# Kernel tuning notes

Measured on AMD Instinct MI355X. Metric: run time of the kernel, lower is better.

The kernel has to match this reference:

```python
import jax, jax.numpy as jnp
import numpy as np
import math

B, S, D, H = 64, 512, 768, 12
HS = D // H  # head size = 64


def setup_inputs() -> dict:
    key = jax.random.key(0)
    ks = jax.random.split(key, 8)
    scale = 1.0 / math.sqrt(D)
    return {
        "from_tensor": jax.random.normal(ks[0], (B, S, D), jnp.float32),
        "to_tensor": jax.random.normal(ks[1], (B, S, D), jnp.float32),
        "Wq": jax.random.normal(ks[2], (D, D), jnp.float32) * scale,
        "bq": jax.random.normal(ks[3], (D,), jnp.float32) * 0.02,
        "Wk": jax.random.normal(ks[4], (D, D), jnp.float32) * scale,
        "bk": jax.random.normal(ks[5], (D,), jnp.float32) * 0.02,
        "Wv": jax.random.normal(ks[6], (D, D), jnp.float32) * scale,
        "bv": jax.random.normal(ks[7], (D,), jnp.float32) * 0.02,
    }


def _split_heads(x):
    # [B, S, D] -> [B, H, S, HS]
    return x.reshape(B, S, H, HS).transpose(0, 2, 1, 3)


def reference(from_tensor, to_tensor, Wq, bq, Wk, bk, Wv, bv):
    q = _split_heads(from_tensor @ Wq + bq)
    k = _split_heads(to_tensor @ Wk + bk)
    v = _split_heads(to_tensor @ Wv + bv)
    scores = jnp.einsum("bhqd,bhkd->bhqk", q, k) / math.sqrt(HS)
    probs = jax.nn.softmax(scores, axis=-1)
    out = jnp.einsum("bhqk,bhkd->bhqd", probs, v)
    return out.transpose(0, 2, 1, 3).reshape(B, S, D)
```

## Files before the change

### kernel.cpp

```cpp
#include <hip/hip_runtime.h>
#include <hip/hip_bf16.h>

#define GAS __attribute__((address_space(1)))
#define LAS __attribute__((address_space(3)))

typedef __attribute__((ext_vector_type(8))) short   bf16x8;
typedef __attribute__((ext_vector_type(4))) float   f32x4;
typedef __attribute__((ext_vector_type(16))) float  f32x16;
typedef __attribute__((ext_vector_type(4))) float   f4;
typedef __attribute__((ext_vector_type(8))) short   s8v;
typedef __attribute__((ext_vector_type(2))) unsigned int u32x2;
typedef __attribute__((ext_vector_type(4))) unsigned int u32x4;

#define NB  64
#define NS  512
#define ND  768
#define NH  12
#define NHS 64
#define NM  (NB*NS)

#define QSCALE 0.18033688011112042f

__device__ __forceinline__ unsigned short f2bf(float x){
  unsigned int u = __float_as_uint(x);
  u += 0x7fffu + ((u >> 16) & 1u);
  return (unsigned short)(u >> 16);
}

__device__ __forceinline__ f32x4 mfma16(bf16x8 a, bf16x8 b, f32x4 c){
  return __builtin_amdgcn_mfma_f32_16x16x32_bf16(a, b, c, 0, 0, 0);
}

__device__ __forceinline__ f32x16 mfma32(bf16x8 a, bf16x8 b, f32x16 c){
  return __builtin_amdgcn_mfma_f32_32x32x16_bf16(a, b, c, 0, 0, 0);
}

__device__ __forceinline__ unsigned int cvtpk(float lo, float hi){
  unsigned int r;
  asm("v_cvt_pk_bf16_f32 %0, %1, %2" : "=v"(r) : "v"(lo), "v"(hi));
  return r;
}

__device__ __forceinline__ bf16x8 u2b(u32x4 u){
  union { u32x4 a; bf16x8 b; } c; c.a = u; return c.b;
}

__global__ void cvt_all(const float* __restrict__ from_t, const float* __restrict__ to_t,
                        const float* __restrict__ Wq, const float* __restrict__ Wk,
                        const float* __restrict__ Wv,
                        short* __restrict__ fb, short* __restrict__ tb,
                        short* __restrict__ Wt){
  int bid = blockIdx.x;
  if (bid < 24576){
    int v = bid * 256 + threadIdx.x;
    const int NG = NM * ND / 8;
    const float* s; short* d;
    if (v < NG){ s = from_t; d = fb; } else { s = to_t; d = tb; v -= NG; }
    f4 a = ((const f4*)s)[(long)v * 2];
    f4 b = ((const f4*)s)[(long)v * 2 + 1];
    s8v o;
    o[0]=(short)f2bf(a[0]); o[1]=(short)f2bf(a[1]); o[2]=(short)f2bf(a[2]); o[3]=(short)f2bf(a[3]);
    o[4]=(short)f2bf(b[0]); o[5]=(short)f2bf(b[1]); o[6]=(short)f2bf(b[2]); o[7]=(short)f2bf(b[3]);
    ((s8v*)d)[v] = o;
  } else {
    int i = (bid - 24576) * 256 + threadIdx.x;
    int mat = i / (ND*ND);
    int rem = i - mat * (ND*ND);
    int k = rem / ND;
    int n = rem - k * ND;
    const float* W = (mat == 0) ? Wq : (mat == 1 ? Wk : Wv);
    Wt[(long)mat*ND*ND + (long)n*ND + k] = (short)f2bf(W[rem]);
  }
}

__global__ __launch_bounds__(512, 2)
void qkv_gemm(const short* __restrict__ Xf, const short* __restrict__ Xt,
              const short* __restrict__ Wt,
              const float* __restrict__ bq, const float* __restrict__ bk,
              const float* __restrict__ bv,
              short* __restrict__ Qw, short* __restrict__ Kw, short* __restrict__ Vtw){
  __shared__ short smem[49152];

  int bid = blockIdx.x;
  int wg  = (bid & 7) * 144 + (bid >> 3);
  int mat = wg / 384;
  int r   = wg - mat * 384;
  int mt  = r / 3;
  int nt  = r - mt * 3;

  const short* A  = (mat == 0) ? Xf : Xt;
  const short* Wp = Wt + (long)mat * ND * ND;

  int t_ = threadIdx.x, wv = t_ >> 6, l = t_ & 63, g = l >> 4, c = l & 15;
  int wm = wv >> 2, wn = wv & 3;
  int m0 = mt * 256, n0 = nt * 256;

  short* As[3] = { smem, smem + 8192, smem + 16384 };
  short* Bs[3] = { smem + 24576, smem + 32768, smem + 40960 };

  auto stage = [&](int kt, short* Ab, short* Bb, int ci){
    int chunk = ci * 8 + wv;
    int ch = chunk & 15;
    int idx = ch * 64 + l;
    int row = idx >> 2, slot = idx & 3;
    int kcol = kt * 32 + ((slot ^ ((row >> 1) & 3)) << 3);
    if (chunk < 16){
      const short* gp = A + (long)(m0 + row) * ND + kcol;
      __builtin_amdgcn_global_load_lds((const GAS unsigned int*)gp,
                                       (LAS unsigned int*)(Ab + ch * 512), 16, 0, 0);
    } else {
      const short* gp = Wp + (long)(n0 + row) * ND + kcol;
      __builtin_amdgcn_global_load_lds((const GAS unsigned int*)gp,
                                       (LAS unsigned int*)(Bb + ch * 512), 16, 0, 0);
    }
  };

  f32x4 zero = {0.f, 0.f, 0.f, 0.f};
  f32x4 acc[8][4];
  #pragma unroll
  for (int i = 0; i < 8; ++i)
    #pragma unroll
    for (int j = 0; j < 4; ++j) acc[i][j] = zero;

  #pragma unroll
  for (int ci = 0; ci < 4; ++ci) stage(0, As[0], Bs[0], ci);
  #pragma unroll
  for (int ci = 0; ci < 4; ++ci) stage(1, As[1], Bs[1], ci);

  auto step = [&](const short* Asl, const short* Bsl, short* An, short* Bn, int t){
    if (t == 23) asm volatile("s_waitcnt vmcnt(0)" ::: "memory");
    else         asm volatile("s_waitcnt vmcnt(4)" ::: "memory");
    __builtin_amdgcn_s_barrier();
    bf16x8 af[8], bfv[4];
    #pragma unroll
    for (int ms = 0; ms < 4; ++ms){
      int row = wm * 128 + ms * 16 + c;
      af[ms] = *(const bf16x8*)(Asl + row * 32 + ((g ^ ((row >> 1) & 3)) << 3));
    }
    if (t < 22) stage(t + 2, An, Bn, 0);
    #pragma unroll
    for (int ns = 0; ns < 4; ++ns){
      int row = wn * 64 + ns * 16 + c;
      bfv[ns] = *(const bf16x8*)(Bsl + row * 32 + ((g ^ ((row >> 1) & 3)) << 3));
    }
    if (t < 22) stage(t + 2, An, Bn, 1);
    #pragma unroll
    for (int ms = 4; ms < 8; ++ms){
      int row = wm * 128 + ms * 16 + c;
      af[ms] = *(const bf16x8*)(Asl + row * 32 + ((g ^ ((row >> 1) & 3)) << 3));
    }
    if (t < 22){ stage(t + 2, An, Bn, 2); stage(t + 2, An, Bn, 3); }
    __builtin_amdgcn_s_setprio(1);
    #pragma unroll
    for (int ms = 0; ms < 8; ++ms)
      #pragma unroll
      for (int ns = 0; ns < 4; ++ns)
        acc[ms][ns] = mfma16(af[ms], bfv[ns], acc[ms][ns]);
    __builtin_amdgcn_s_setprio(0);
  };

  for (int it = 0; it < 8; ++it){
    int t = it * 3;
    step(As[0], Bs[0], As[2], Bs[2], t);
    step(As[1], Bs[1], As[0], Bs[0], t + 1);
    step(As[2], Bs[2], As[1], Bs[1], t + 2);
  }

  __builtin_amdgcn_s_barrier();

  int n0g = n0 + wn * 64;
  const float* bias = (mat == 0) ? bq : (mat == 1 ? bk : bv);
  float bb[4];
  #pragma unroll
  for (int ns = 0; ns < 4; ++ns) bb[ns] = bias[n0g + ns * 16 + c];
  short* chunk = smem + wv * 4096;
  int hq = n0g >> 6;

  if (mat < 2){
    short* O = (mat == 0) ? Qw : Kw;
    float scl = (mat == 0) ? QSCALE : 1.0f;
    #pragma unroll
    for (int sp = 0; sp < 2; ++sp){
      #pragma unroll
      for (int msl = 0; msl < 4; ++msl){
        #pragma unroll
        for (int ns = 0; ns < 4; ++ns){
          int col = ns * 16 + c;
          #pragma unroll
          for (int i = 0; i < 4; ++i){
            int row = msl * 16 + g * 4 + i;
            chunk[row * 64 + (((col >> 3) ^ (row & 7)) << 3) + (col & 7)] =
                (short)f2bf((acc[sp * 4 + msl][ns][i] + bb[ns]) * scl);
          }
        }
      }
      asm volatile("s_waitcnt lgkmcnt(0)" ::: "memory");
      __builtin_amdgcn_sched_barrier(0);
      #pragma unroll
      for (int rr = 0; rr < 8; ++rr){
        int row = rr * 8 + (l >> 3);
        int slot = l & 7;
        bf16x8 v = *(const bf16x8*)(chunk + row * 64 + ((slot ^ (row & 7)) << 3));
        int m = m0 + wm * 128 + sp * 64 + row;
        int b = m >> 9, s2 = m & 511;
        *(bf16x8*)(O + (((long)(b * NH + hq) * NS + s2) << 6) + slot * 8) = v;
      }
      if (sp == 0){ asm volatile("s_waitcnt lgkmcnt(0)" ::: "memory"); }
    }
  } else {
    #pragma unroll
    for (int sp = 0; sp < 2; ++sp){
      #pragma unroll
      for (int msl = 0; msl < 4; ++msl){
        #pragma unroll
        for (int ns = 0; ns < 4; ++ns){
          int hs = ns * 16 + c;
          #pragma unroll
          for (int i = 0; i < 4; ++i){
            int col = msl * 16 + g * 4 + i;
            chunk[hs * 64 + (((col >> 3) ^ (hs & 7)) << 3) + (col & 7)] =
                (short)f2bf(acc[sp * 4 + msl][ns][i] + bb[ns]);
          }
        }
      }
      asm volatile("s_waitcnt lgkmcnt(0)" ::: "memory");
      __builtin_amdgcn_sched_barrier(0);
      int mbase = m0 + wm * 128 + sp * 64;
      int b = mbase >> 9, s0 = mbase & 511;
      #pragma unroll
      for (int rr = 0; rr < 8; ++rr){
        int hs = rr * 8 + (l >> 3);
        int slot = l & 7;
        bf16x8 v = *(const bf16x8*)(chunk + hs * 64 + ((slot ^ (hs & 7)) << 3));
        *(bf16x8*)(Vtw + (long)((b * NH + hq) * 64 + hs) * NS + s0 + slot * 8) = v;
      }
      if (sp == 0){ asm volatile("s_waitcnt lgkmcnt(0)" ::: "memory"); }
    }
  }
}

__global__ __launch_bounds__(512, 1)
void attn_kernel(const short* __restrict__ Qw, const short* __restrict__ Kw,
                 const short* __restrict__ Vtw, float* __restrict__ out){
  extern __shared__ char smem[];
  short* Ks = (short*)smem;
  short* Vs = (short*)(smem + 65536);

  int bh = blockIdx.x;
  int t = threadIdx.x, wv = t >> 6, l = t & 63;
  int lam = l & 31, hi = l >> 5;
  int r7 = lam & 7;

  const short* Kb = Kw  + (long)bh * NS * NHS;
  const short* Vb = Vtw + (long)bh * NS * NHS;

  #pragma unroll
  for (int it = 0; it < 8; ++it){
    int chunk = it * 8 + wv;
    {
      int idx = chunk * 64 + l;
      int row = idx >> 3, slot = idx & 7;
      const short* gk = Kb + row * 64 + ((slot ^ (row & 7)) * 8);
      __builtin_amdgcn_global_load_lds((const GAS unsigned int*)gk,
                                       (LAS unsigned int*)(Ks + chunk * 512), 16, 0, 0);
    }
    {
      int row = chunk, slot = l;
      const short* gv = Vb + (long)row * NS + (((slot & 56) | ((slot & 7) ^ (row & 7))) * 8);
      __builtin_amdgcn_global_load_lds((const GAS unsigned int*)gv,
                                       (LAS unsigned int*)(Vs + chunk * 512), 16, 0, 0);
    }
  }
  __syncthreads();

  int b = bh / NH, h = bh - b * NH;
  float* outb = out + (long)b * NS * ND + (long)h * 64;

  for (int qt = 0; qt < 2; ++qt){
    int q0 = wv * 64 + qt * 32;
    const short* Qb = Qw + (((long)bh * NS + q0 + lam) << 6) + hi * 8;
    bf16x8 qf[4];
    #pragma unroll
    for (int dk = 0; dk < 4; ++dk) qf[dk] = *(const bf16x8*)(Qb + dk * 16);

    f32x16 o0, o1;
    #pragma unroll
    for (int j = 0; j < 16; ++j){ o0[j] = 0.f; o1[j] = 0.f; }
    float m_run = -1e30f, lsum = 0.f;

    f32x16 s2[2];
    bf16x8 kfr[2][4];
    {
      const char* kb = (const char*)Ks + lam * 128;
      #pragma unroll
      for (int dk = 0; dk < 4; ++dk)
        kfr[0][dk] = *(const bf16x8*)(kb + (((hi + 2 * dk) ^ r7) << 4));
      #pragma unroll
      for (int j = 0; j < 16; ++j) s2[0][j] = 0.f;
      __builtin_amdgcn_s_setprio(1);
      #pragma unroll
      for (int dk = 0; dk < 4; ++dk) s2[0] = mfma32(kfr[0][dk], qf[dk], s2[0]);
      __builtin_amdgcn_s_setprio(0);
    }

    #pragma unroll
    for (int ch = 0; ch < 16; ++ch){
      const int cur = ch & 1, nxt = cur ^ 1;

      if (ch < 15){
        const char* kb = (const char*)Ks + ((ch + 1) * 32 + lam) * 128;
        #pragma unroll
        for (int dk = 0; dk < 4; ++dk)
          kfr[nxt][dk] = *(const bf16x8*)(kb + (((hi + 2 * dk) ^ r7) << 4));
      }

      float t8[8], t4[4];
      #pragma unroll
      for (int j = 0; j < 8; ++j) t8[j] = fmaxf(s2[cur][j], s2[cur][j + 8]);
      #pragma unroll
      for (int j = 0; j < 4; ++j) t4[j] = fmaxf(t8[j], t8[j + 4]);
      float m1 = fmaxf(fmaxf(t4[0], t4[1]), fmaxf(t4[2], t4[3]));
      float pmax = fmaxf(m1, __shfl_xor(m1, 32));
      if (__any(pmax > m_run + 8.0f)){
        float mnew = fmaxf(m_run, pmax);
        float cf = exp2f(m_run - mnew);
        lsum *= cf;
        #pragma unroll
        for (int j = 0; j < 16; ++j){ o0[j] *= cf; o1[j] *= cf; }
        m_run = mnew;
      }
      float p[16];
      #pragma unroll
      for (int j = 0; j < 16; ++j) p[j] = exp2f(s2[cur][j] - m_run);
      float a8[8], a4[4];
      #pragma unroll
      for (int j = 0; j < 8; ++j) a8[j] = p[j] + p[j + 8];
      #pragma unroll
      for (int j = 0; j < 4; ++j) a4[j] = a8[j] + a8[j + 4];
      lsum += (a4[0] + a4[1]) + (a4[2] + a4[3]);

      if (ch < 15){
        #pragma unroll
        for (int j = 0; j < 16; ++j) s2[nxt][j] = 0.f;
        __builtin_amdgcn_s_setprio(1);
        #pragma unroll
        for (int dk = 0; dk < 4; ++dk) s2[nxt] = mfma32(kfr[nxt][dk], qf[dk], s2[nxt]);
        __builtin_amdgcn_s_setprio(0);
      }

      unsigned int w[8];
      #pragma unroll
      for (int rr = 0; rr < 8; ++rr) w[rr] = cvtpk(p[2 * rr], p[2 * rr + 1]);
      unsigned int y0 = (unsigned int)__shfl_xor((int)(hi ? w[0] : w[2]), 32);
      unsigned int y1 = (unsigned int)__shfl_xor((int)(hi ? w[1] : w[3]), 32);
      unsigned int y2 = (unsigned int)__shfl_xor((int)(hi ? w[4] : w[6]), 32);
      unsigned int y3 = (unsigned int)__shfl_xor((int)(hi ? w[5] : w[7]), 32);
      u32x4 fa, fb;
      if (hi){
        fa[0] = y0;   fa[1] = y1;   fa[2] = w[2]; fa[3] = w[3];
        fb[0] = y2;   fb[1] = y3;   fb[2] = w[6]; fb[3] = w[7];
      } else {
        fa[0] = w[0]; fa[1] = w[1]; fa[2] = y0;   fa[3] = y1;
        fb[0] = w[4]; fb[1] = w[5]; fb[2] = y2;   fb[3] = y3;
      }
      bf16x8 pa = u2b(fa), pb = u2b(fb);

      const char* vb0 = (const char*)Vs + lam * 1024;
      const char* vb1 = (const char*)Vs + (32 + lam) * 1024;
      int sl0 = ch * 4 + hi, sl1 = ch * 4 + 2 + hi;
      int sw0 = ((sl0 & 56) | ((sl0 & 7) ^ r7)) << 4;
      int sw1 = ((sl1 & 56) | ((sl1 & 7) ^ r7)) << 4;
      bf16x8 v00 = *(const bf16x8*)(vb0 + sw0);
      bf16x8 v01 = *(const bf16x8*)(vb0 + sw1);
      bf16x8 v10 = *(const bf16x8*)(vb1 + sw0);
      bf16x8 v11 = *(const bf16x8*)(vb1 + sw1);
      __builtin_amdgcn_s_setprio(1);
      o0 = mfma32(v00, pa, o0);
      o0 = mfma32(v01, pb, o0);
      o1 = mfma32(v10, pa, o1);
      o1 = mfma32(v11, pb, o1);
      __builtin_amdgcn_s_setprio(0);
    }

    float lt = lsum + __shfl_xor(lsum, 32);
    float invl = 1.0f / lt;
    float* orow = outb + (long)(q0 + lam) * ND;
    #pragma unroll
    for (int r = 0; r < 4; ++r){
      f4 u0, u1;
      #pragma unroll
      for (int jj = 0; jj < 4; ++jj){
        u0[jj] = o0[4 * r + jj] * invl;
        u1[jj] = o1[4 * r + jj] * invl;
      }
      *(f4*)(orow + 4 * hi + 8 * r)      = u0;
      *(f4*)(orow + 32 + 4 * hi + 8 * r) = u1;
    }
  }
}

extern "C" void kernel_launch(void* const* d_in, const int* in_sizes, int n_in,
                              void* d_out, int out_size, void* d_ws, size_t ws_size,
                              hipStream_t stream){
  const float* from_t = (const float*)d_in[0];
  const float* to_t   = (const float*)d_in[1];
  const float* Wq = (const float*)d_in[2];
  const float* bq = (const float*)d_in[3];
  const float* Wk = (const float*)d_in[4];
  const float* bk = (const float*)d_in[5];
  const float* Wv = (const float*)d_in[6];
  const float* bv = (const float*)d_in[7];

  short* fb  = (short*)d_ws;
  short* tb  = fb  + 25165824;
  short* Wt  = tb  + 25165824;
  short* Qw  = Wt  + 1769472;
  short* Kw  = Qw  + 25165824;
  short* Vtw = Kw  + 25165824;

  cvt_all<<<31488, 256, 0, stream>>>(from_t, to_t, Wq, Wk, Wv, fb, tb, Wt);
  qkv_gemm<<<1152, 512, 0, stream>>>(fb, tb, Wt, bq, bk, bv, Qw, Kw, Vtw);
  attn_kernel<<<768, 512, 131072, stream>>>(Qw, Kw, Vtw, (float*)d_out);
}
```

Measured before the change: 323.1 us.

## Fuse fp32-to-bf16 activation conversion into the QKV GEMM A-operand load

The GEMM now streams the fp32 activations directly into LDS with an XOR swizzle. It converts them to bf16 in registers, using packed converts, while building the MFMA A fragments. This removes the separate conversion pass and its bf16 intermediate buffers, which cost an extra read and write of both input tensors. In exchange the GEMM loads twice as many A bytes per tile, grows LDS use to 144KB per block, and issues more global-to-LDS loads per step. Each A tile is also reconverted by all three N-tile blocks.

```diff
diff --git a/kernel.cpp b/kernel.cpp
--- a/kernel.cpp
+++ b/kernel.cpp
@@ -9,7 +9,6 @@
 typedef __attribute__((ext_vector_type(16))) float  f32x16;
 typedef __attribute__((ext_vector_type(4))) float   f4;
 typedef __attribute__((ext_vector_type(8))) short   s8v;
-typedef __attribute__((ext_vector_type(2))) unsigned int u32x2;
 typedef __attribute__((ext_vector_type(4))) unsigned int u32x4;
 
 #define NB  64
@@ -45,41 +44,24 @@
   union { u32x4 a; bf16x8 b; } c; c.a = u; return c.b;
 }
 
-__global__ void cvt_all(const float* __restrict__ from_t, const float* __restrict__ to_t,
-                        const float* __restrict__ Wq, const float* __restrict__ Wk,
-                        const float* __restrict__ Wv,
-                        short* __restrict__ fb, short* __restrict__ tb,
-                        short* __restrict__ Wt){
-  int bid = blockIdx.x;
-  if (bid < 24576){
-    int v = bid * 256 + threadIdx.x;
-    const int NG = NM * ND / 8;
-    const float* s; short* d;
-    if (v < NG){ s = from_t; d = fb; } else { s = to_t; d = tb; v -= NG; }
-    f4 a = ((const f4*)s)[(long)v * 2];
-    f4 b = ((const f4*)s)[(long)v * 2 + 1];
-    s8v o;
-    o[0]=(short)f2bf(a[0]); o[1]=(short)f2bf(a[1]); o[2]=(short)f2bf(a[2]); o[3]=(short)f2bf(a[3]);
-    o[4]=(short)f2bf(b[0]); o[5]=(short)f2bf(b[1]); o[6]=(short)f2bf(b[2]); o[7]=(short)f2bf(b[3]);
-    ((s8v*)d)[v] = o;
-  } else {
-    int i = (bid - 24576) * 256 + threadIdx.x;
-    int mat = i / (ND*ND);
-    int rem = i - mat * (ND*ND);
-    int k = rem / ND;
-    int n = rem - k * ND;
-    const float* W = (mat == 0) ? Wq : (mat == 1 ? Wk : Wv);
-    Wt[(long)mat*ND*ND + (long)n*ND + k] = (short)f2bf(W[rem]);
-  }
+__global__ void cvt_w(const float* __restrict__ Wq, const float* __restrict__ Wk,
+                      const float* __restrict__ Wv, short* __restrict__ Wt){
+  int i = blockIdx.x * 256 + threadIdx.x;
+  int mat = i / (ND*ND);
+  int rem = i - mat * (ND*ND);
+  int k = rem / ND;
+  int n = rem - k * ND;
+  const float* W = (mat == 0) ? Wq : (mat == 1 ? Wk : Wv);
+  Wt[(long)mat*ND*ND + (long)n*ND + k] = (short)f2bf(W[rem]);
 }
 
 __global__ __launch_bounds__(512, 2)
-void qkv_gemm(const short* __restrict__ Xf, const short* __restrict__ Xt,
+void qkv_gemm(const float* __restrict__ from_t, const float* __restrict__ to_t,
               const short* __restrict__ Wt,
               const float* __restrict__ bq, const float* __restrict__ bk,
               const float* __restrict__ bv,
               short* __restrict__ Qw, short* __restrict__ Kw, short* __restrict__ Vtw){
-  __shared__ short smem[49152];
+  __shared__ short smem[73728];
 
   int bid = blockIdx.x;
   int wg  = (bid & 7) * 144 + (bid >> 3);
@@ -88,31 +70,38 @@
   int mt  = r / 3;
   int nt  = r - mt * 3;
 
-  const short* A  = (mat == 0) ? Xf : Xt;
+  const float* Af = (mat == 0) ? from_t : to_t;
   const short* Wp = Wt + (long)mat * ND * ND;
 
   int t_ = threadIdx.x, wv = t_ >> 6, l = t_ & 63, g = l >> 4, c = l & 15;
   int wm = wv >> 2, wn = wv & 3;
   int m0 = mt * 256, n0 = nt * 256;
 
-  short* As[3] = { smem, smem + 8192, smem + 16384 };
-  short* Bs[3] = { smem + 24576, smem + 32768, smem + 40960 };
-
-  auto stage = [&](int kt, short* Ab, short* Bb, int ci){
+  auto stage = [&](int kt, int sl, int ci){
     int chunk = ci * 8 + wv;
-    int ch = chunk & 15;
-    int idx = ch * 64 + l;
-    int row = idx >> 2, slot = idx & 3;
-    int kcol = kt * 32 + ((slot ^ ((row >> 1) & 3)) << 3);
-    if (chunk < 16){
-      const short* gp = A + (long)(m0 + row) * ND + kcol;
+    if (chunk < 32){
+      int idx = chunk * 64 + l;
+      int row = idx >> 3, slot = idx & 7;
+      const float* gp = Af + (long)(m0 + row) * ND + kt * 32 + ((slot ^ (row & 7)) << 2);
       __builtin_amdgcn_global_load_lds((const GAS unsigned int*)gp,
-                                       (LAS unsigned int*)(Ab + ch * 512), 16, 0, 0);
+                                       (LAS unsigned int*)(smem + sl * 16384 + idx * 8), 16, 0, 0);
     } else {
-      const short* gp = Wp + (long)(n0 + row) * ND + kcol;
+      int idx = (chunk - 32) * 64 + l;
+      int row = idx >> 2, slot = idx & 3;
+      const short* gp = Wp + (long)(n0 + row) * ND + kt * 32 + ((slot ^ ((row >> 1) & 3)) << 3);
       __builtin_amdgcn_global_load_lds((const GAS unsigned int*)gp,
-                                       (LAS unsigned int*)(Bb + ch * 512), 16, 0, 0);
-    }
+                                       (LAS unsigned int*)(smem + 49152 + sl * 8192 + idx * 8), 16, 0, 0);
+    }
+  };
+
+  auto ldA = [&](const short* Asl, int row) -> bf16x8 {
+    const char* base = (const char*)Asl + row * 128;
+    f4 lo = *(const f4*)(base + (((2 * g)     ^ (row & 7)) << 4));
+    f4 hi = *(const f4*)(base + (((2 * g + 1) ^ (row & 7)) << 4));
+    u32x4 pk;
+    pk[0] = cvtpk(lo[0], lo[1]); pk[1] = cvtpk(lo[2], lo[3]);
+    pk[2] = cvtpk(hi[0], hi[1]); pk[3] = cvtpk(hi[2], hi[3]);
+    return u2b(pk);
   };
 
   f32x4 zero = {0.f, 0.f, 0.f, 0.f};
@@ -123,33 +112,31 @@
     for (int j = 0; j < 4; ++j) acc[i][j] = zero;
 
   #pragma unroll
-  for (int ci = 0; ci < 4; ++ci) stage(0, As[0], Bs[0], ci);
+  for (int ci = 0; ci < 6; ++ci) stage(0, 0, ci);
   #pragma unroll
-  for (int ci = 0; ci < 4; ++ci) stage(1, As[1], Bs[1], ci);
-
-  auto step = [&](const short* Asl, const short* Bsl, short* An, short* Bn, int t){
+  for (int ci = 0; ci < 6; ++ci) stage(1, 1, ci);
+
+  auto step = [&](int sl, int sl2, int t){
+    const short* Asl = smem + sl * 16384;
+    const short* Bsl = smem + 49152 + sl * 8192;
     if (t == 23) asm volatile("s_waitcnt vmcnt(0)" ::: "memory");
-    else         asm volatile("s_waitcnt vmcnt(4)" ::: "memory");
+    else         asm volatile("s_waitcnt vmcnt(6)" ::: "memory");
     __builtin_amdgcn_s_barrier();
     bf16x8 af[8], bfv[4];
     #pragma unroll
-    for (int ms = 0; ms < 4; ++ms){
-      int row = wm * 128 + ms * 16 + c;
-      af[ms] = *(const bf16x8*)(Asl + row * 32 + ((g ^ ((row >> 1) & 3)) << 3));
-    }
-    if (t < 22) stage(t + 2, An, Bn, 0);
+    for (int ms = 0; ms < 4; ++ms)
+      af[ms] = ldA(Asl, wm * 128 + ms * 16 + c);
+    if (t < 22){ stage(t + 2, sl2, 0); stage(t + 2, sl2, 1); }
     #pragma unroll
     for (int ns = 0; ns < 4; ++ns){
       int row = wn * 64 + ns * 16 + c;
       bfv[ns] = *(const bf16x8*)(Bsl + row * 32 + ((g ^ ((row >> 1) & 3)) << 3));
     }
-    if (t < 22) stage(t + 2, An, Bn, 1);
-    #pragma unroll
-    for (int ms = 4; ms < 8; ++ms){
-      int row = wm * 128 + ms * 16 + c;
-      af[ms] = *(const bf16x8*)(Asl + row * 32 + ((g ^ ((row >> 1) & 3)) << 3));
-    }
-    if (t < 22){ stage(t + 2, An, Bn, 2); stage(t + 2, An, Bn, 3); }
+    if (t < 22){ stage(t + 2, sl2, 2); stage(t + 2, sl2, 3); }
+    #pragma unroll
+    for (int ms = 4; ms < 8; ++ms)
+      af[ms] = ldA(Asl, wm * 128 + ms * 16 + c);
+    if (t < 22){ stage(t + 2, sl2, 4); stage(t + 2, sl2, 5); }
     __builtin_amdgcn_s_setprio(1);
     #pragma unroll
     for (int ms = 0; ms < 8; ++ms)
@@ -161,9 +148,9 @@
 
   for (int it = 0; it < 8; ++it){
     int t = it * 3;
-    step(As[0], Bs[0], As[2], Bs[2], t);
-    step(As[1], Bs[1], As[0], Bs[0], t + 1);
-    step(As[2], Bs[2], As[1], Bs[1], t + 2);
+    step(0, 2, t);
+    step(1, 0, t + 1);
+    step(2, 1, t + 2);
   }
 
   __builtin_amdgcn_s_barrier();
@@ -411,14 +398,12 @@
   const float* Wv = (const float*)d_in[6];
   const float* bv = (const float*)d_in[7];
 
-  short* fb  = (short*)d_ws;
-  short* tb  = fb  + 25165824;
-  short* Wt  = tb  + 25165824;
+  short* Wt  = (short*)d_ws;
   short* Qw  = Wt  + 1769472;
   short* Kw  = Qw  + 25165824;
   short* Vtw = Kw  + 25165824;
 
-  cvt_all<<<31488, 256, 0, stream>>>(from_t, to_t, Wq, Wk, Wv, fb, tb, Wt);
-  qkv_gemm<<<1152, 512, 0, stream>>>(fb, tb, Wt, bq, bk, bv, Qw, Kw, Vtw);
+  cvt_w<<<6912, 256, 0, stream>>>(Wq, Wk, Wv, Wt);
+  qkv_gemm<<<1152, 512, 0, stream>>>(from_t, to_t, Wt, bq, bk, bv, Qw, Kw, Vtw);
   attn_kernel<<<768, 512, 131072, stream>>>(Qw, Kw, Vtw, (float*)d_out);
 }
```

After: 305.2 us. 5.5% less time.
